# Kernel tuning notes

Hardware: AMD Instinct MI355X
Metric: run time of the kernel (lower is better)

## Reference

```python
import jax, jax.numpy as jnp
import numpy as np

EMBED = 512
COS_TAU = 0.3          # cosine temperature in CrossModalAttention
SOFT_TAU = 0.3         # soft_mask_tau in TokenSparse
SPARSE_RATIO = 0.6     # keep ratio
SCALE = EMBED ** -0.5


def setup_inputs() -> dict:
    key = jax.random.key(0)
    ks = jax.random.split(key, 18)
    B, N, C = 64, 256, 512
    W = 0.02  # param init scale
    return {
        "rgb": jax.random.normal(ks[0], (B, N, C), jnp.float32),
        "nir": jax.random.normal(ks[1], (B, N, C), jnp.float32),
        "tir": jax.random.normal(ks[2], (B, N, C), jnp.float32),
        "rgb_g": jax.random.normal(ks[3], (B, C), jnp.float32),
        "nir_g": jax.random.normal(ks[4], (B, C), jnp.float32),
        "tir_g": jax.random.normal(ks[5], (B, C), jnp.float32),
        # 9 CrossModalAttention modules in order:
        # rgb_self, rgb_cross_nir, rgb_cross_tir,
        # nir_self, nir_cross_rgb, nir_cross_tir,
        # tir_self, tir_cross_rgb, tir_cross_nir
        "attn_qw": jax.random.normal(ks[6], (9, C, C), jnp.float32) * W,
        "attn_qb": jnp.zeros((9, C), jnp.float32),
        "attn_kw": jax.random.normal(ks[7], (9, C, C), jnp.float32) * W,
        "attn_kb": jnp.zeros((9, C), jnp.float32),
        # 3 TokenSparse adaptive-weight MLPs (rgb, nir, tir)
        "mlp_w1": jax.random.normal(ks[8], (3, 3 * C, 256), jnp.float32) * W,
        "mlp_b1": jnp.zeros((3, 256), jnp.float32),
        "ln_g": jnp.ones((3, 256), jnp.float32),
        "ln_b": jnp.zeros((3, 256), jnp.float32),
        "mlp_w2": jax.random.normal(ks[9], (3, 256, 64), jnp.float32) * W,
        "mlp_b2": jnp.zeros((3, 64), jnp.float32),
        "mlp_w3": jax.random.normal(ks[10], (3, 64, 3), jnp.float32) * W,
        "mlp_b3": jnp.zeros((3, 3), jnp.float32),
    }


def _cosine(p, g):
    # F.cosine_similarity(patches, global.unsqueeze(1), dim=-1) -> (B, N)
    pn = p / jnp.maximum(jnp.linalg.norm(p, axis=-1, keepdims=True), 1e-8)
    gn = g / jnp.maximum(jnp.linalg.norm(g, axis=-1, keepdims=True), 1e-8)
    return jnp.einsum('bnc,bc->bn', pn, gn)


def _attn_score(patches, g, qw, qb, kw, kb):
    # single-head cross-attention: softmax(q k^T / sqrt(C) + cos / tau)
    cos = _cosine(patches, g)
    q = g @ qw + qb                         # (B, C)
    k = jnp.einsum('bnc,cd->bnd', patches, kw) + kb  # (B, N, C)
    logits = jnp.einsum('bc,bnc->bn', q, k) * SCALE + cos / COS_TAU
    return jax.nn.softmax(logits, axis=-1)


def _norm_score(s):
    # z-score (unbiased std like torch.std) + sigmoid
    m = jnp.mean(s, axis=-1, keepdims=True)
    sd = jnp.std(s, axis=-1, ddof=1, keepdims=True) + 1e-5
    return jax.nn.sigmoid((s - m) / sd)


def _layernorm(x, g, b):
    m = jnp.mean(x, axis=-1, keepdims=True)
    v = jnp.var(x, axis=-1, keepdims=True)
    return (x - m) / jnp.sqrt(v + 1e-5) * g + b


def _token_sparse(tokens, s_im, s_m2, s_m3, gfeats, w1, b1, lg, lb, w2, b2, w3, b3):
    s_im, s_m2, s_m3 = _norm_score(s_im), _norm_score(s_m2), _norm_score(s_m3)
    h = jax.nn.gelu(_layernorm(gfeats @ w1 + b1, lg, lb), approximate=False)
    h = jax.nn.gelu(h @ w2 + b2, approximate=False)
    w = jax.nn.softmax(h @ w3 + b3, axis=-1)            # (B, 3)
    score = w[:, 0:1] * s_im + w[:, 1:2] * s_m2 + w[:, 2:3] * s_m3
    thr = jnp.quantile(score, 1.0 - SPARSE_RATIO, axis=1, keepdims=True)
    mask = jax.nn.sigmoid((score - thr) / SOFT_TAU)     # (B, N)
    return tokens * mask[..., None], mask


def reference(rgb, nir, tir, rgb_g, nir_g, tir_g,
              attn_qw, attn_qb, attn_kw, attn_kb,
              mlp_w1, mlp_b1, ln_g, ln_b, mlp_w2, mlp_b2, mlp_w3, mlp_b3):
    patches = (rgb, nir, tir)
    globs = (rgb_g, nir_g, tir_g)
    # guide modality indices per target modality: (self, other1, other2)
    guides = ((0, 1, 2), (1, 0, 2), (2, 0, 1))
    gcat = jnp.concatenate([rgb_g, nir_g, tir_g], axis=-1)  # (B, 3C)
    outs, masks = [], []
    for mi in range(3):
        p = patches[mi]
        s = [
            _attn_score(p, globs[g],
                        attn_qw[3 * mi + j], attn_qb[3 * mi + j],
                        attn_kw[3 * mi + j], attn_kb[3 * mi + j])
            for j, g in enumerate(guides[mi])
        ]
        mt, mk = _token_sparse(p, s[0], s[1], s[2], gcat,
                               mlp_w1[mi], mlp_b1[mi], ln_g[mi], ln_b[mi],
                               mlp_w2[mi], mlp_b2[mi], mlp_w3[mi], mlp_b3[mi])
        outs.append(mt)
        masks.append(mk)
    return (outs[0], outs[1], outs[2], masks[0], masks[1], masks[2])
```

## Files before the change

kernel.cpp:

```cpp
#include <hip/hip_runtime.h>
#include <math.h>

#define B 64
#define N 256
#define C 512

typedef float nfloat4 __attribute__((ext_vector_type(4)));

__device__ __forceinline__ int guide_of(int m) {
    int mi = m / 3, j = m % 3;
    return (j == 0) ? mi : (j == 1 ? ((mi == 0) ? 1 : 0) : ((mi == 2) ? 1 : 2));
}

template<int NW>
__device__ __forceinline__ float breduce_sum(float v, volatile float* red, int t) {
    int w = t >> 6, l = t & 63;
#pragma unroll
    for (int mm = 1; mm < 64; mm <<= 1) v += __shfl_xor(v, mm);
    __syncthreads();
    if (l == 0) red[w] = v;
    __syncthreads();
    float s = red[0];
#pragma unroll
    for (int i = 1; i < NW; i++) s += red[i];
    return s;
}

template<int NW>
__device__ __forceinline__ float breduce_max(float v, volatile float* red, int t) {
    int w = t >> 6, l = t & 63;
#pragma unroll
    for (int mm = 1; mm < 64; mm <<= 1) v = fmaxf(v, __shfl_xor(v, mm));
    __syncthreads();
    if (l == 0) red[w] = v;
    __syncthreads();
    float s = red[0];
#pragma unroll
    for (int i = 1; i < NW; i++) s = fmaxf(s, red[i]);
    return s;
}

__device__ __forceinline__ float dot4(float4 a, float4 b) {
    return a.x * b.x + a.y * b.y + a.z * b.z + a.w * b.w;
}

__global__ __launch_bounds__(256) void k_proj_mlp(const float* g0, const float* g1, const float* g2,
                                                  const float* qw, const float* w1,
                                                  float* part, float* h1part) {
    int bid = blockIdx.x;
    int t = threadIdx.x;
    __shared__ float gt[64 * 128];
    if (bid < 576) {
        int cx = bid & 7, m = (bid >> 3) % 9, ks = bid / 72;
        int c0 = cx * 64, e0 = ks * 64;
        int gi = guide_of(m);
        const float* g = (gi == 0) ? g0 : (gi == 1 ? g1 : g2);
        for (int idx = t; idx < 1024; idx += 256) {
            int r = idx >> 4, c4 = idx & 15;
            ((float4*)&gt[r * 128])[c4] = ((const float4*)(g + (size_t)r * C + e0))[c4];
        }
        __syncthreads();
        int c = c0 + (t & 63);
        int br = (t >> 6) * 16;
        float acc[16];
#pragma unroll
        for (int i = 0; i < 16; i++) acc[i] = 0.f;
        const float* W = qw + (size_t)m * C * C + (size_t)e0 * C + c;
#pragma unroll 4
        for (int e = 0; e < 64; e++) {
            float wv = W[(size_t)e * C];
#pragma unroll
            for (int i = 0; i < 16; i++) acc[i] += gt[(br + i) * 128 + e] * wv;
        }
#pragma unroll
        for (int i = 0; i < 16; i++)
            part[(size_t)ks * 294912 + ((size_t)m * B + br + i) * C + c] = acc[i];
    } else {
        int r = bid - 576;
        int cx = r & 3, mi = (r >> 2) % 3, ks = r / 12;
        int e0 = ks * 128;
        const float* g = (e0 < 512) ? g0 : (e0 < 1024 ? g1 : g2);
        int eo = e0 & 511;
        for (int idx = t; idx < 2048; idx += 256) {
            int rr = idx >> 5, c4 = idx & 31;
            ((float4*)&gt[rr * 128])[c4] = ((const float4*)(g + (size_t)rr * C + eo))[c4];
        }
        __syncthreads();
        int c = cx * 64 + (t & 63);
        int br = (t >> 6) * 16;
        float acc[16];
#pragma unroll
        for (int i = 0; i < 16; i++) acc[i] = 0.f;
        const float* W = w1 + ((size_t)mi * 1536 + e0) * 256 + c;
#pragma unroll 4
        for (int e = 0; e < 128; e++) {
            float wv = W[(size_t)e * 256];
#pragma unroll
            for (int i = 0; i < 16; i++) acc[i] += gt[(br + i) * 128 + e] * wv;
        }
#pragma unroll
        for (int i = 0; i < 16; i++)
            h1part[(((size_t)ks * 3 + mi) * B + br + i) * 256 + c] = acc[i];
    }
}

__global__ __launch_bounds__(256) void k_kproj(const float* kw, const float* part,
                                               const float* qb, const float* kb,
                                               float* kpart, float* qkb_part) {
    int cx = blockIdx.x, m = blockIdx.y, ds = blockIdx.z;
    int t = threadIdx.x;
    int c0 = cx * 64, d0 = ds * 64;
    __shared__ float kt[64][65];
    __shared__ float qt[64][64];
    for (int idx = t; idx < 1024; idx += 256) {
        int r = idx >> 4, c4 = idx & 15;
        float4 kv4 = *(const float4*)(kw + ((size_t)m * C + c0 + r) * C + d0 + c4 * 4);
        kt[r][c4 * 4 + 0] = kv4.x; kt[r][c4 * 4 + 1] = kv4.y;
        kt[r][c4 * 4 + 2] = kv4.z; kt[r][c4 * 4 + 3] = kv4.w;
        float4 s = *(const float4*)(qb + (size_t)m * C + d0 + c4 * 4);
        const float* pp = part + ((size_t)m * B + r) * C + d0 + c4 * 4;
#pragma unroll
        for (int ks = 0; ks < 8; ks++) {
            float4 v = *(const float4*)(pp + (size_t)ks * 294912);
            s.x += v.x; s.y += v.y; s.z += v.z; s.w += v.w;
        }
        ((float4*)qt[r])[c4] = s;
    }
    __syncthreads();
    int c = t & 63;
    int br = (t >> 6) * 16;
    float acc[16];
#pragma unroll
    for (int i = 0; i < 16; i++) acc[i] = 0.f;
#pragma unroll 4
    for (int d = 0; d < 64; d++) {
        float kv = kt[c][d];
#pragma unroll
        for (int i = 0; i < 16; i++) acc[i] += kv * qt[br + i][d];
    }
#pragma unroll
    for (int i = 0; i < 16; i++)
        kpart[(size_t)ds * 294912 + ((size_t)m * B + br + i) * C + c0 + c] = acc[i];
    if (cx == 0 && t < 64) {
        float s = 0.f;
        const float* kbp = kb + (size_t)m * C + d0;
        for (int d = 0; d < 64; d++) s += qt[t][d] * kbp[d];
        qkb_part[((size_t)m * 8 + ds) * B + t] = s;
    }
}

__global__ __launch_bounds__(256) void k_logits(const float* p0, const float* p1, const float* p2,
                                                const float* kpart, const float* qkb_part,
                                                const float* g0, const float* g1, const float* g2,
                                                float* lgt) {
    int b = blockIdx.x, mi = blockIdx.y, ns = blockIdx.z;
    int t = threadIdx.x, w = t >> 6, l = t & 63;
    const float* p = (mi == 0) ? p0 : (mi == 1 ? p1 : p2);
    __shared__ float q6[6][512];
    __shared__ float ginv_s[3];
    __shared__ float qkb_s[3];
    for (int idx = t; idx < 768; idx += 256) {
        int row = idx >> 7, c4 = idx & 127;
        float4 v;
        if (row < 3) {
            int m = 3 * mi + row;
            const float4* kp = (const float4*)kpart + ((size_t)m * B + b) * 128 + c4;
            v = kp[0];
#pragma unroll
            for (int ds = 1; ds < 8; ds++) {
                float4 u = kp[(size_t)ds * 73728];
                v.x += u.x; v.y += u.y; v.z += u.z; v.w += u.w;
            }
        } else {
            int gi = guide_of(3 * mi + row - 3);
            const float* graw = (gi == 0) ? g0 : (gi == 1 ? g1 : g2);
            v = ((const float4*)(graw + (size_t)b * C))[c4];
        }
        ((float4*)q6[row])[c4] = v;
    }
    if (t < 3) {
        int m = 3 * mi + t;
        float s = 0.f;
#pragma unroll
        for (int ds = 0; ds < 8; ds++) s += qkb_part[((size_t)m * 8 + ds) * B + b];
        qkb_s[t] = s;
    }
    __syncthreads();
    if (w < 3) {
        const float4* r4 = (const float4*)q6[3 + w];
        float4 a = r4[l * 2], bb = r4[l * 2 + 1];
        float n2 = dot4(a, a) + dot4(bb, bb);
#pragma unroll
        for (int mm = 1; mm < 64; mm <<= 1) n2 += __shfl_xor(n2, mm);
        if (l == 0) ginv_s[w] = 1.0f / fmaxf(sqrtf(n2), 1e-8f);
    }
    __syncthreads();
    float qkbv[3];
#pragma unroll
    for (int j = 0; j < 3; j++) qkbv[j] = qkb_s[j];
    const float4* pbase = (const float4*)(p + (size_t)b * N * C);
    const float SCALE = 0.044194173824159216f;
    float* L = lgt + (size_t)(mi * B + b) * 3 * N;
    int s = l & 7, tl = l >> 3;
    const float4* Q0 = (const float4*)q6[0];
    const float4* Q1 = (const float4*)q6[1];
    const float4* Q2 = (const float4*)q6[2];
    const float4* G0 = (const float4*)q6[3];
    const float4* G1 = (const float4*)q6[4];
    const float4* G2 = (const float4*)q6[5];
    {
        int n = ns * 32 + w * 8 + tl;
        const float4* prow = pbase + (size_t)n * 128;
        float pp = 0.f, dj0 = 0.f, dj1 = 0.f, dj2 = 0.f, cj0 = 0.f, cj1 = 0.f, cj2 = 0.f;
#pragma unroll
        for (int i = 0; i < 16; i++) {
            int o = s + 8 * i;
            float4 pv = prow[o];
            pp  += dot4(pv, pv);
            dj0 += dot4(pv, Q0[o]);
            dj1 += dot4(pv, Q1[o]);
            dj2 += dot4(pv, Q2[o]);
            cj0 += dot4(pv, G0[o]);
            cj1 += dot4(pv, G1[o]);
            cj2 += dot4(pv, G2[o]);
        }
#pragma unroll
        for (int mm = 1; mm < 8; mm <<= 1) {
            pp  += __shfl_xor(pp, mm);
            dj0 += __shfl_xor(dj0, mm);
            dj1 += __shfl_xor(dj1, mm);
            dj2 += __shfl_xor(dj2, mm);
            cj0 += __shfl_xor(cj0, mm);
            cj1 += __shfl_xor(cj1, mm);
            cj2 += __shfl_xor(cj2, mm);
        }
        if (s == 0) {
            float rn = fmaxf(sqrtf(pp), 1e-8f);
            float ic = 1.0f / (rn * 0.3f);
            L[0 * N + n] = (dj0 + qkbv[0]) * SCALE + cj0 * ginv_s[0] * ic;
            L[1 * N + n] = (dj1 + qkbv[1]) * SCALE + cj1 * ginv_s[1] * ic;
            L[2 * N + n] = (dj2 + qkbv[2]) * SCALE + cj2 * ginv_s[2] * ic;
        }
    }
}

__global__ __launch_bounds__(256) void k_finscale(const float* lgt, const float* h1part,
                                                  const float* b1, const float* lng, const float* lnb,
                                                  const float* w2, const float* b2,
                                                  const float* w3, const float* b3,
                                                  const float* p0, const float* p1, const float* p2,
                                                  float* out) {
    int b = blockIdx.x, mi = blockIdx.y, ns = blockIdx.z, t = threadIdx.x;
    __shared__ float h1[256];
    __shared__ float h2p[4][64];
    __shared__ float h2[64];
    __shared__ float red[4];
    __shared__ float wjs[3];
    __shared__ float sc[256];
    __shared__ float mks[256];
    __shared__ float thr_s;
    float a1 = b1[mi * 256 + t];
#pragma unroll
    for (int ks = 0; ks < 12; ks++) a1 += h1part[(((size_t)ks * 3 + mi) * B + b) * 256 + t];
    float total = breduce_sum<4>(a1, red, t);
    float mean = total * (1.0f / 256.0f);
    float dv = a1 - mean;
    float vtot = breduce_sum<4>(dv * dv, red, t);
    float var = vtot * (1.0f / 256.0f);
    float x = dv / sqrtf(var + 1e-5f) * lng[mi * 256 + t] + lnb[mi * 256 + t];
    x = 0.5f * x * (1.0f + erff(x * 0.70710678118654752f));
    h1[t] = x;
    __syncthreads();
    {
        int col = t & 63, sl = t >> 6;
        float a2 = 0.f;
        const float* W2 = w2 + (size_t)mi * 256 * 64 + col;
#pragma unroll 8
        for (int e = sl * 64; e < sl * 64 + 64; e++) a2 += h1[e] * W2[(size_t)e * 64];
        h2p[sl][col] = a2;
    }
    __syncthreads();
    if (t < 64) {
        float a2 = b2[mi * 64 + t];
#pragma unroll
        for (int s2 = 0; s2 < 4; s2++) a2 += h2p[s2][t];
        a2 = 0.5f * a2 * (1.0f + erff(a2 * 0.70710678118654752f));
        h2[t] = a2;
    }
    __syncthreads();
    if (t == 0) {
        float l3[3];
        for (int j = 0; j < 3; j++) {
            float a3 = b3[mi * 3 + j];
            for (int e = 0; e < 64; e++) a3 += h2[e] * w3[((size_t)mi * 64 + e) * 3 + j];
            l3[j] = a3;
        }
        float mx = fmaxf(l3[0], fmaxf(l3[1], l3[2]));
        float e0 = expf(l3[0] - mx), e1 = expf(l3[1] - mx), e2 = expf(l3[2] - mx);
        float inv = 1.0f / (e0 + e1 + e2);
        wjs[0] = e0 * inv; wjs[1] = e1 * inv; wjs[2] = e2 * inv;
    }
    __syncthreads();
    const float* L = lgt + (size_t)(mi * B + b) * 3 * N;
    float score = 0.f;
    for (int j = 0; j < 3; j++) {
        float v = L[j * N + t];
        float mx = breduce_max<4>(v, red, t);
        float e = expf(v - mx);
        float s = breduce_sum<4>(e, red, t);
        float pr = e / s;
        float tot2 = breduce_sum<4>(pr, red, t);
        float mean2 = tot2 * (1.0f / 256.0f);
        float dv2 = pr - mean2;
        float vtot2 = breduce_sum<4>(dv2 * dv2, red, t);
        float sd = sqrtf(vtot2 * (1.0f / 255.0f)) + 1e-5f;
        float z = dv2 / sd;
        float sg = 1.0f / (1.0f + expf(-z));
        score += wjs[j] * sg;
    }
    sc[t] = score;
    __syncthreads();
    {
        int cl = 0, ce = 0;
        for (int m2 = 0; m2 < N; m2++) {
            float v2 = sc[m2];
            cl += (v2 < score) ? 1 : 0;
            ce += (v2 == score) ? 1 : 0;
        }
        if (cl <= 102 && 102 < cl + ce) thr_s = score;
    }
    __syncthreads();
    float thr = thr_s;
    float mk = 1.0f / (1.0f + expf(-(score - thr) * (1.0f / 0.3f)));
    mks[t] = mk;
    if ((t >> 5) == ns)
        out[(size_t)3 * B * N * C + ((size_t)mi * B + b) * N + t] = mk;
    __syncthreads();
    const float* p = (mi == 0) ? p0 : (mi == 1 ? p1 : p2);
    const nfloat4* pslab = (const nfloat4*)(p + (size_t)b * N * C + (size_t)ns * 32 * C);
    nfloat4* oslab = (nfloat4*)(out + (size_t)mi * B * N * C + (size_t)b * N * C
                                + (size_t)ns * 32 * C);
#pragma unroll 4
    for (int idx = t; idx < 4096; idx += 256) {
        nfloat4 v = __builtin_nontemporal_load(pslab + idx);
        float mkv = mks[ns * 32 + (idx >> 7)];
        v.x *= mkv; v.y *= mkv; v.z *= mkv; v.w *= mkv;
        __builtin_nontemporal_store(v, oslab + idx);
    }
}

extern "C" void kernel_launch(void* const* d_in, const int* in_sizes, int n_in,
                              void* d_out, int out_size, void* d_ws, size_t ws_size,
                              hipStream_t stream) {
    const float* rgb   = (const float*)d_in[0];
    const float* nir   = (const float*)d_in[1];
    const float* tir   = (const float*)d_in[2];
    const float* rgb_g = (const float*)d_in[3];
    const float* nir_g = (const float*)d_in[4];
    const float* tir_g = (const float*)d_in[5];
    const float* attn_qw = (const float*)d_in[6];
    const float* attn_qb = (const float*)d_in[7];
    const float* attn_kw = (const float*)d_in[8];
    const float* attn_kb = (const float*)d_in[9];
    const float* mlp_w1 = (const float*)d_in[10];
    const float* mlp_b1 = (const float*)d_in[11];
    const float* ln_g = (const float*)d_in[12];
    const float* ln_b = (const float*)d_in[13];
    const float* mlp_w2 = (const float*)d_in[14];
    const float* mlp_b2 = (const float*)d_in[15];
    const float* mlp_w3 = (const float*)d_in[16];
    const float* mlp_b3 = (const float*)d_in[17];
    float* out = (float*)d_out;

    float* ws = (float*)d_ws;
    float* part     = ws;
    float* kpart    = ws + 2359296;
    float* qkb_part = ws + 4718592;
    float* h1part   = ws + 4723712;
    float* lgt      = ws + 5313536;

    k_proj_mlp<<<720, 256, 0, stream>>>(rgb_g, nir_g, tir_g, attn_qw, mlp_w1, part, h1part);
    k_kproj<<<dim3(8, 9, 8), 256, 0, stream>>>(attn_kw, part, attn_qb, attn_kb, kpart, qkb_part);
    k_logits<<<dim3(B, 3, 8), 256, 0, stream>>>(rgb, nir, tir, kpart, qkb_part,
                                                rgb_g, nir_g, tir_g, lgt);
    k_finscale<<<dim3(B, 3, 8), 256, 0, stream>>>(lgt, h1part, mlp_b1, ln_g, ln_b,
                                                  mlp_w2, mlp_b2, mlp_w3, mlp_b3,
                                                  rgb, nir, tir, out);
}
```

Measured before the change: 115.5 us.

## Use 4x4 register tiles with float4 weights in projections; precompute normalized globals

The q-projection, MLP first layer and k-projection GEMM kernels move from one-column-by-16-rows accumulation to 4x4 register tiles. Each thread now does float4 weight loads and float4 stores, and the shared rows are padded to reduce bank conflicts. Three extra blocks in the first kernel normalize the global vectors once and write them to the workspace. The logits kernel then reads those pre-normalized vectors instead of recomputing the norm in each of 1536 blocks, which also removes a sync. The risks are different LDS access patterns and a small added workspace dependency.

Result: faster. 109.9 us (-4.8%).

```diff
diff --git a/kernel.cpp b/kernel.cpp
--- a/kernel.cpp
+++ b/kernel.cpp
@@ -46,36 +46,40 @@
 
 __global__ __launch_bounds__(256) void k_proj_mlp(const float* g0, const float* g1, const float* g2,
                                                   const float* qw, const float* w1,
-                                                  float* part, float* h1part) {
+                                                  float* part, float* h1part, float* gn) {
     int bid = blockIdx.x;
     int t = threadIdx.x;
-    __shared__ float gt[64 * 128];
+    __shared__ float gt[64 * 132];
     if (bid < 576) {
         int cx = bid & 7, m = (bid >> 3) % 9, ks = bid / 72;
-        int c0 = cx * 64, e0 = ks * 64;
+        int e0 = ks * 64;
         int gi = guide_of(m);
         const float* g = (gi == 0) ? g0 : (gi == 1 ? g1 : g2);
         for (int idx = t; idx < 1024; idx += 256) {
             int r = idx >> 4, c4 = idx & 15;
-            ((float4*)&gt[r * 128])[c4] = ((const float4*)(g + (size_t)r * C + e0))[c4];
+            ((float4*)&gt[r * 132])[c4] = ((const float4*)(g + (size_t)r * C + e0))[c4];
         }
         __syncthreads();
-        int c = c0 + (t & 63);
-        int br = (t >> 6) * 16;
-        float acc[16];
-#pragma unroll
-        for (int i = 0; i < 16; i++) acc[i] = 0.f;
-        const float* W = qw + (size_t)m * C * C + (size_t)e0 * C + c;
+        int c0 = cx * 64 + 4 * (t & 15);
+        int b0 = 4 * (t >> 4);
+        float4 acc[4];
+#pragma unroll
+        for (int j = 0; j < 4; j++) acc[j] = make_float4(0.f, 0.f, 0.f, 0.f);
+        const float* W = qw + (size_t)m * C * C + (size_t)e0 * C + c0;
 #pragma unroll 4
         for (int e = 0; e < 64; e++) {
-            float wv = W[(size_t)e * C];
-#pragma unroll
-            for (int i = 0; i < 16; i++) acc[i] += gt[(br + i) * 128 + e] * wv;
-        }
-#pragma unroll
-        for (int i = 0; i < 16; i++)
-            part[(size_t)ks * 294912 + ((size_t)m * B + br + i) * C + c] = acc[i];
-    } else {
+            float4 wv = *(const float4*)(W + (size_t)e * C);
+#pragma unroll
+            for (int j = 0; j < 4; j++) {
+                float gv = gt[(b0 + j) * 132 + e];
+                acc[j].x += gv * wv.x; acc[j].y += gv * wv.y;
+                acc[j].z += gv * wv.z; acc[j].w += gv * wv.w;
+            }
+        }
+#pragma unroll
+        for (int j = 0; j < 4; j++)
+            *(float4*)(part + (size_t)ks * 294912 + ((size_t)m * B + b0 + j) * C + c0) = acc[j];
+    } else if (bid < 720) {
         int r = bid - 576;
         int cx = r & 3, mi = (r >> 2) % 3, ks = r / 12;
         int e0 = ks * 128;
@@ -83,24 +87,44 @@
         int eo = e0 & 511;
         for (int idx = t; idx < 2048; idx += 256) {
             int rr = idx >> 5, c4 = idx & 31;
-            ((float4*)&gt[rr * 128])[c4] = ((const float4*)(g + (size_t)rr * C + eo))[c4];
+            ((float4*)&gt[rr * 132])[c4] = ((const float4*)(g + (size_t)rr * C + eo))[c4];
         }
         __syncthreads();
-        int c = cx * 64 + (t & 63);
-        int br = (t >> 6) * 16;
-        float acc[16];
-#pragma unroll
-        for (int i = 0; i < 16; i++) acc[i] = 0.f;
-        const float* W = w1 + ((size_t)mi * 1536 + e0) * 256 + c;
+        int c0 = cx * 64 + 4 * (t & 15);
+        int b0 = 4 * (t >> 4);
+        float4 acc[4];
+#pragma unroll
+        for (int j = 0; j < 4; j++) acc[j] = make_float4(0.f, 0.f, 0.f, 0.f);
+        const float* W = w1 + ((size_t)mi * 1536 + e0) * 256 + c0;
 #pragma unroll 4
         for (int e = 0; e < 128; e++) {
-            float wv = W[(size_t)e * 256];
-#pragma unroll
-            for (int i = 0; i < 16; i++) acc[i] += gt[(br + i) * 128 + e] * wv;
-        }
-#pragma unroll
-        for (int i = 0; i < 16; i++)
-            h1part[(((size_t)ks * 3 + mi) * B + br + i) * 256 + c] = acc[i];
+            float4 wv = *(const float4*)(W + (size_t)e * 256);
+#pragma unroll
+            for (int j = 0; j < 4; j++) {
+                float gv = gt[(b0 + j) * 132 + e];
+                acc[j].x += gv * wv.x; acc[j].y += gv * wv.y;
+                acc[j].z += gv * wv.z; acc[j].w += gv * wv.w;
+            }
+        }
+#pragma unroll
+        for (int j = 0; j < 4; j++)
+            *(float4*)(h1part + (((size_t)ks * 3 + mi) * B + b0 + j) * 256 + c0) = acc[j];
+    } else {
+        int gm = bid - 720;
+        const float* g = (gm == 0) ? g0 : (gm == 1 ? g1 : g2);
+        int wv = t >> 6, l = t & 63;
+        for (int r = wv; r < 64; r += 4) {
+            const float4* gv = (const float4*)(g + (size_t)r * C);
+            float4 a = gv[l], b2 = gv[64 + l];
+            float n2 = dot4(a, a) + dot4(b2, b2);
+#pragma unroll
+            for (int mm = 1; mm < 64; mm <<= 1) n2 += __shfl_xor(n2, mm);
+            float inv = 1.0f / fmaxf(sqrtf(n2), 1e-8f);
+            float4* o = (float4*)(gn + ((size_t)gm * B + r) * C);
+            a.x *= inv; a.y *= inv; a.z *= inv; a.w *= inv;
+            b2.x *= inv; b2.y *= inv; b2.z *= inv; b2.w *= inv;
+            o[l] = a; o[64 + l] = b2;
+        }
     }
 }
 
@@ -109,12 +133,12 @@
                                                float* kpart, float* qkb_part) {
     int cx = blockIdx.x, m = blockIdx.y, ds = blockIdx.z;
     int t = threadIdx.x;
-    int c0 = cx * 64, d0 = ds * 64;
+    int c0b = cx * 64, d0 = ds * 64;
     __shared__ float kt[64][65];
-    __shared__ float qt[64][64];
+    __shared__ float qt[64][65];
     for (int idx = t; idx < 1024; idx += 256) {
         int r = idx >> 4, c4 = idx & 15;
-        float4 kv4 = *(const float4*)(kw + ((size_t)m * C + c0 + r) * C + d0 + c4 * 4);
+        float4 kv4 = *(const float4*)(kw + ((size_t)m * C + c0b + r) * C + d0 + c4 * 4);
         kt[r][c4 * 4 + 0] = kv4.x; kt[r][c4 * 4 + 1] = kv4.y;
         kt[r][c4 * 4 + 2] = kv4.z; kt[r][c4 * 4 + 3] = kv4.w;
         float4 s = *(const float4*)(qb + (size_t)m * C + d0 + c4 * 4);
@@ -124,23 +148,28 @@
             float4 v = *(const float4*)(pp + (size_t)ks * 294912);
             s.x += v.x; s.y += v.y; s.z += v.z; s.w += v.w;
         }
-        ((float4*)qt[r])[c4] = s;
-    }
-    __syncthreads();
-    int c = t & 63;
-    int br = (t >> 6) * 16;
-    float acc[16];
-#pragma unroll
-    for (int i = 0; i < 16; i++) acc[i] = 0.f;
+        qt[r][c4 * 4 + 0] = s.x; qt[r][c4 * 4 + 1] = s.y;
+        qt[r][c4 * 4 + 2] = s.z; qt[r][c4 * 4 + 3] = s.w;
+    }
+    __syncthreads();
+    int c0 = 4 * (t & 15);
+    int b0 = 4 * (t >> 4);
+    float4 acc[4];
+#pragma unroll
+    for (int j = 0; j < 4; j++) acc[j] = make_float4(0.f, 0.f, 0.f, 0.f);
 #pragma unroll 4
     for (int d = 0; d < 64; d++) {
-        float kv = kt[c][d];
-#pragma unroll
-        for (int i = 0; i < 16; i++) acc[i] += kv * qt[br + i][d];
-    }
-#pragma unroll
-    for (int i = 0; i < 16; i++)
-        kpart[(size_t)ds * 294912 + ((size_t)m * B + br + i) * C + c0 + c] = acc[i];
+        float k0 = kt[c0 + 0][d], k1 = kt[c0 + 1][d], k2 = kt[c0 + 2][d], k3 = kt[c0 + 3][d];
+#pragma unroll
+        for (int j = 0; j < 4; j++) {
+            float qv = qt[b0 + j][d];
+            acc[j].x += qv * k0; acc[j].y += qv * k1;
+            acc[j].z += qv * k2; acc[j].w += qv * k3;
+        }
+    }
+#pragma unroll
+    for (int j = 0; j < 4; j++)
+        *(float4*)(kpart + (size_t)ds * 294912 + ((size_t)m * B + b0 + j) * C + c0b + c0) = acc[j];
     if (cx == 0 && t < 64) {
         float s = 0.f;
         const float* kbp = kb + (size_t)m * C + d0;
@@ -151,13 +180,11 @@
 
 __global__ __launch_bounds__(256) void k_logits(const float* p0, const float* p1, const float* p2,
                                                 const float* kpart, const float* qkb_part,
-                                                const float* g0, const float* g1, const float* g2,
-                                                float* lgt) {
+                                                const float* gn, float* lgt) {
     int b = blockIdx.x, mi = blockIdx.y, ns = blockIdx.z;
     int t = threadIdx.x, w = t >> 6, l = t & 63;
     const float* p = (mi == 0) ? p0 : (mi == 1 ? p1 : p2);
     __shared__ float q6[6][512];
-    __shared__ float ginv_s[3];
     __shared__ float qkb_s[3];
     for (int idx = t; idx < 768; idx += 256) {
         int row = idx >> 7, c4 = idx & 127;
@@ -173,8 +200,7 @@
             }
         } else {
             int gi = guide_of(3 * mi + row - 3);
-            const float* graw = (gi == 0) ? g0 : (gi == 1 ? g1 : g2);
-            v = ((const float4*)(graw + (size_t)b * C))[c4];
+            v = ((const float4*)(gn + ((size_t)gi * B + b) * C))[c4];
         }
         ((float4*)q6[row])[c4] = v;
     }
@@ -184,15 +210,6 @@
 #pragma unroll
         for (int ds = 0; ds < 8; ds++) s += qkb_part[((size_t)m * 8 + ds) * B + b];
         qkb_s[t] = s;
-    }
-    __syncthreads();
-    if (w < 3) {
-        const float4* r4 = (const float4*)q6[3 + w];
-        float4 a = r4[l * 2], bb = r4[l * 2 + 1];
-        float n2 = dot4(a, a) + dot4(bb, bb);
-#pragma unroll
-        for (int mm = 1; mm < 64; mm <<= 1) n2 += __shfl_xor(n2, mm);
-        if (l == 0) ginv_s[w] = 1.0f / fmaxf(sqrtf(n2), 1e-8f);
     }
     __syncthreads();
     float qkbv[3];
@@ -237,9 +254,9 @@
         if (s == 0) {
             float rn = fmaxf(sqrtf(pp), 1e-8f);
             float ic = 1.0f / (rn * 0.3f);
-            L[0 * N + n] = (dj0 + qkbv[0]) * SCALE + cj0 * ginv_s[0] * ic;
-            L[1 * N + n] = (dj1 + qkbv[1]) * SCALE + cj1 * ginv_s[1] * ic;
-            L[2 * N + n] = (dj2 + qkbv[2]) * SCALE + cj2 * ginv_s[2] * ic;
+            L[0 * N + n] = (dj0 + qkbv[0]) * SCALE + cj0 * ic;
+            L[1 * N + n] = (dj1 + qkbv[1]) * SCALE + cj1 * ic;
+            L[2 * N + n] = (dj2 + qkbv[2]) * SCALE + cj2 * ic;
         }
     }
 }
@@ -378,11 +395,13 @@
     float* qkb_part = ws + 4718592;
     float* h1part   = ws + 4723712;
     float* lgt      = ws + 5313536;
-
-    k_proj_mlp<<<720, 256, 0, stream>>>(rgb_g, nir_g, tir_g, attn_qw, mlp_w1, part, h1part);
-    k_kproj<<<dim3(8, 9, 8), 256, 0, stream>>>(attn_kw, part, attn_qb, attn_kb, kpart, qkb_part);
-    k_logits<<<dim3(B, 3, 8), 256, 0, stream>>>(rgb, nir, tir, kpart, qkb_part,
-                                                rgb_g, nir_g, tir_g, lgt);
+    float* gn       = ws + 5460992;
+
+    k_proj_mlp<<<723, 256, 0, stream>>>(rgb_g, nir_g, tir_g, attn_qw, mlp_w1,
+                                        part, h1part, gn);
+    k_kproj<<<dim3(8, 9, 8), 256, 0, stream>>>(attn_kw, part, attn_qb, attn_kb,
+                                               kpart, qkb_part);
+    k_logits<<<dim3(B, 3, 8), 256, 0, stream>>>(rgb, nir, tir, kpart, qkb_part, gn, lgt);
     k_finscale<<<dim3(B, 3, 8), 256, 0, stream>>>(lgt, h1part, mlp_b1, ln_g, ln_b,
                                                   mlp_w2, mlp_b2, mlp_w3, mlp_b3,
                                                   rgb, nir, tir, out);
```
